# Kernel optimization log

Measured on AMD Instinct MI355X. Metric: run time of the kernel, lower is better.

Reference implementation:

```python
import jax, jax.numpy as jnp
import numpy as np

# Config mirroring MultiHeadAttention1d(in_channels=256, n_heads=8, residual=False,
# kernel_size=1, attention_type=0) applied to 3-D inputs (B, C, N).
B, C, N, H, D = 4, 256, 2048, 8, 256  # per-head dim D = in_channels; OC = H*D = 2048
OC = H * D


def setup_inputs() -> dict:
    key = jax.random.key(0)
    ks = jax.random.split(key, 14)
    s = 1.0 / np.sqrt(C)
    f32 = jnp.float32
    inp = {
        "x": jax.random.normal(ks[0], (B, C, N), f32),
        "y": jax.random.normal(ks[1], (B, C, N), f32),
        # ConvNormActivation1d (kernel_size=1) == pointwise conv + (folded, eval-mode)
        # BatchNorm affine + ReLU. BN folds to per-channel scale g and shift beta.
        "Wq": jax.random.normal(ks[2], (OC, C), f32) * s,
        "bq": jax.random.normal(ks[3], (OC,), f32) * 0.01,
        "gq": jnp.ones((OC,), f32),
        "betaq": jnp.zeros((OC,), f32),
        "Wk": jax.random.normal(ks[4], (OC, C), f32) * s,
        "bk": jax.random.normal(ks[5], (OC,), f32) * 0.01,
        "gk": jnp.ones((OC,), f32),
        "betak": jnp.zeros((OC,), f32),
        "Wv": jax.random.normal(ks[6], (OC, C), f32) * s,
        "bv": jax.random.normal(ks[7], (OC,), f32) * 0.01,
        "gv": jnp.ones((OC,), f32),
        "betav": jnp.zeros((OC,), f32),
    }
    return inp


def _cna(W, b, g, beta, t):
    # 1x1 conv (channel GEMM) + folded-BN affine + ReLU; t: (B, C, N) -> (B, OC, N)
    z = jnp.einsum("oc,bcn->bon", W, t) + b[:, None]
    return jax.nn.relu(g[:, None] * z + beta[:, None])


def _heads(t):
    # (B, OC, N) -> (B, H, N, D); channel split matches torch.split chunks of size D
    return t.reshape(B, H, D, N).transpose(0, 1, 3, 2)


def reference(x, y, Wq, bq, gq, betaq, Wk, bk, gk, betak, Wv, bv, gv, betav):
    q = _heads(_cna(Wq, bq, gq, betaq, x))  # (B,H,N,D)
    k = _heads(_cna(Wk, bk, gk, betak, y))
    v = _heads(_cna(Wv, bv, gv, betav, y))
    energy = jnp.einsum("bhnd,bhmd->bhnm", q, k)  # bmm(Q, K^T)
    attn = jax.nn.softmax(energy, axis=-1)
    out = jnp.einsum("bhnm,bhmd->bhnd", attn, v)  # (B,H,N,D)
    # torch path: view(H,B,k,N,D).permute(1,0,3,2,4) -> (B,H,N,k=1,D);
    # squeeze(dim=2) is a no-op since N != 1.
    return out[:, :, :, None, :]  # (B, H, N, 1, D)
```

## Files before the change

kernel.cpp:

```cpp
#include <hip/hip_runtime.h>
#include <cstdint>
#include <cstddef>

typedef unsigned short u16;
typedef __attribute__((ext_vector_type(4))) float f32x4;
typedef __attribute__((ext_vector_type(16))) float f32x16;
typedef __attribute__((ext_vector_type(8))) _Float16 f16x8;
typedef __attribute__((ext_vector_type(4))) u16   u16x4;
typedef __attribute__((ext_vector_type(8))) u16   u16x8;
typedef __attribute__((ext_vector_type(4))) int   i32x4;

#define DEV static __device__ __forceinline__
#define MFMA16(a,b,c) __builtin_amdgcn_mfma_f32_16x16x32_f16((a),(b),(c),0,0,0)
#define MFMA32(a,b,c) __builtin_amdgcn_mfma_f32_32x32x16_f16((a),(b),(c),0,0,0)

constexpr int Bc = 4, Cc = 256, Nc = 2048, Hc = 8, Dc = 256, OCc = 2048;

constexpr size_t OFF_XT = 0;
constexpr size_t OFF_YT = OFF_XT + (size_t)Bc*Nc*Cc*2;
constexpr size_t OFF_WQ = OFF_YT + (size_t)Bc*Nc*Cc*2;
constexpr size_t OFF_WK = OFF_WQ + (size_t)OCc*Cc*2;
constexpr size_t OFF_WV = OFF_WK + (size_t)OCc*Cc*2;
constexpr size_t OFF_BQ = OFF_WV + (size_t)OCc*Cc*2;
constexpr size_t OFF_BK = OFF_BQ + (size_t)OCc*4;
constexpr size_t OFF_BV = OFF_BK + (size_t)OCc*4;
constexpr size_t OFF_Q  = OFF_BV + (size_t)OCc*4;
constexpr size_t OFF_K  = OFF_Q  + (size_t)Bc*Hc*Nc*Dc*2;
constexpr size_t OFF_V  = OFF_K  + (size_t)Bc*Hc*Nc*Dc*2;

DEV u16 f2h(float x){
  _Float16 h = (_Float16)x;
  return __builtin_bit_cast(u16, h);
}

DEV void load_lds16(const void* g, void* l){
  __builtin_amdgcn_global_load_lds((const __attribute__((address_space(1))) int*)g,
                                   (__attribute__((address_space(3))) int*)l, 16, 0, 0);
}

__global__ __launch_bounds__(256) void transpose_cast(const float* __restrict__ x,
                                                      const float* __restrict__ y,
                                                      u16* __restrict__ XT,
                                                      u16* __restrict__ YT){
  __shared__ u16 tile[64][65];
  int b = blockIdx.z >> 1;
  const float* src = (blockIdx.z & 1) ? y : x;
  u16* dst = (blockIdx.z & 1) ? YT : XT;
  int n0 = blockIdx.x * 64, c0 = blockIdx.y * 64;
  int t = threadIdx.x;
#pragma unroll
  for (int i = 0; i < 16; ++i){
    int slot = i*256 + t;
    int cl = slot >> 6, nl = slot & 63;
    tile[cl][nl] = f2h(src[((size_t)b*Cc + c0 + cl)*Nc + n0 + nl]);
  }
  __syncthreads();
#pragma unroll
  for (int i = 0; i < 8; ++i){
    int slot = i*256 + t;
    int nl = slot >> 5, cl = (slot & 31)*2;
    uint32_t v = (uint32_t)tile[cl][nl] | ((uint32_t)tile[cl+1][nl] << 16);
    *(uint32_t*)(dst + ((size_t)b*Nc + n0 + nl)*Cc + c0 + cl) = v;
  }
}

__global__ __launch_bounds__(256) void prep_w(const float* __restrict__ W,
                                              const float* __restrict__ bsrc,
                                              const float* __restrict__ g,
                                              const float* __restrict__ beta,
                                              u16* __restrict__ Wo,
                                              float* __restrict__ bb){
  int idx = (blockIdx.x*256 + threadIdx.x) * 8;
  int o = idx >> 8, c = idx & 255;
  float gg = g[o];
  f32x4 a0 = *(const f32x4*)(W + idx);
  f32x4 a1 = *(const f32x4*)(W + idx + 4);
  u16x8 r;
#pragma unroll
  for (int i = 0; i < 4; ++i){ r[i] = f2h(a0[i]*gg); r[i+4] = f2h(a1[i]*gg); }
  *(u16x8*)(Wo + idx) = r;
  if (c == 0) bb[o] = gg*bsrc[o] + beta[o];
}

template<int SW>
__global__ __launch_bounds__(256, 2) void proj_gemm(const u16* __restrict__ Xt,
                                                    const u16* __restrict__ Wp,
                                                    const float* __restrict__ bb,
                                                    u16* __restrict__ outp){
  __shared__ __align__(16) char lds[32768];
  int t = threadIdx.x, w = t >> 6, l = t & 63, q = l & 15, g = l >> 4;
  int b = blockIdx.z;
  int n0 = blockIdx.x * 128, o0 = blockIdx.y * 128;
  int fs = ((q >> 1) & 3) << 4;
  int partg = ((l & 3) ^ ((l >> 3) & 3));
  f32x4 acc[4][4] = {};

  for (int it = 0; it < 4; ++it){
    __syncthreads();
#pragma unroll
    for (int j = 0; j < 8; ++j){
      int s = j*4 + w;
      int chunk = s >> 3;
      int off = (s & 7) * 1024;
      int row = (s & 7)*16 + (l >> 2);
      const char* gsrc;
      if (chunk < 2)
        gsrc = (const char*)(Wp + (size_t)(o0 + row)*Cc) + it*128 + chunk*64 + partg*16;
      else
        gsrc = (const char*)(Xt + ((size_t)b*Nc + n0 + row)*Cc) + it*128 + (chunk & 1)*64 + partg*16;
      load_lds16(gsrc, lds + chunk*8192 + off);
    }
    asm volatile("s_waitcnt vmcnt(0)" ::: "memory");
    __syncthreads();
#pragma unroll
    for (int kc = 0; kc < 2; ++kc){
      f16x8 fw[4], fx[4];
#pragma unroll
      for (int i = 0; i < 4; ++i){
        int wrow = (SW ? (w & 1) : (w >> 1))*64 + i*16 + q;
        int xrow = (SW ? (w >> 1) : (w & 1))*64 + i*16 + q;
        fw[i] = *(const f16x8*)(lds + kc*8192 + wrow*64 + ((g*16) ^ fs));
        fx[i] = *(const f16x8*)(lds + 16384 + kc*8192 + xrow*64 + ((g*16) ^ fs));
      }
#pragma unroll
      for (int i = 0; i < 4; ++i)
#pragma unroll
        for (int jj = 0; jj < 4; ++jj){
          if constexpr (!SW) acc[i][jj] = MFMA16(fw[i], fx[jj], acc[i][jj]);
          else               acc[i][jj] = MFMA16(fx[i], fw[jj], acc[i][jj]);
        }
    }
  }

  if constexpr (!SW) {
    f32x4 bias[4];
#pragma unroll
    for (int i = 0; i < 4; ++i) bias[i] = *(const f32x4*)(bb + o0 + (w>>1)*64 + i*16 + 4*g);
#pragma unroll
    for (int i = 0; i < 4; ++i)
#pragma unroll
      for (int jj = 0; jj < 4; ++jj){
        u16x4 pk;
#pragma unroll
        for (int r = 0; r < 4; ++r){
          float z = acc[i][jj][r] + bias[i][r];
          pk[r] = f2h(fmaxf(z, 0.f));
        }
        int o = o0 + (w>>1)*64 + i*16 + 4*g;
        int n = n0 + (w&1)*64 + jj*16 + q;
        int hh = o >> 8, d = o & 255;
        *(u16x4*)(outp + ((size_t)((b*Hc + hh)*Nc + n))*Dc + d) = pk;
      }
  } else {
    float biasv[4];
#pragma unroll
    for (int i = 0; i < 4; ++i) biasv[i] = bb[o0 + (w&1)*64 + i*16 + q];
#pragma unroll
    for (int i = 0; i < 4; ++i)
#pragma unroll
      for (int jj = 0; jj < 4; ++jj){
        u16x4 pk;
#pragma unroll
        for (int r = 0; r < 4; ++r){
          float z = acc[i][jj][r] + biasv[jj];
          pk[r] = f2h(fmaxf(z, 0.f));
        }
        int o = o0 + (w&1)*64 + jj*16 + q;
        int n = n0 + (w>>1)*64 + i*16 + 4*g;
        int hh = o >> 8, d = o & 255;
        *(u16x4*)(outp + ((size_t)((b*Hc + hh)*Dc + d))*Nc + n) = pk;
      }
  }
}

__global__ __launch_bounds__(512, 1) void attn_kernel(const u16* __restrict__ Qp,
                                                      const u16* __restrict__ Kp,
                                                      const u16* __restrict__ Vp,
                                                      float* __restrict__ outp){
  __shared__ __align__(16) char lds[150528];
  const int t = threadIdx.x, w = t >> 6, l = t & 63, lq = l & 31, hi = l >> 5;
  const int wq = w & 3, wm = w >> 2;
  const int h = blockIdx.y, b = blockIdx.z;
  const int q0 = blockIdx.x * 128;
  size_t head = (size_t)(b*Hc + h) * Nc * Dc;
  const u16* Qh = Qp + head;
  const u16* Kh = Kp + head;
  const u16* Vh = Vp + head;

  char* Pex  = lds + 131072;
  float* smax = (float*)(lds + 147456);
  float* ssum = (float*)(lds + 148480);
  float* sscl = (float*)(lds + 149504);
  float* slinv= (float*)(lds + 150016);

  f16x8 qf[16];
  {
    const u16* qrow = Qh + (size_t)(q0 + wq*32 + lq) * Dc;
#pragma unroll
    for (int kc = 0; kc < 16; ++kc) qf[kc] = *(const f16x8*)(qrow + kc*16 + hi*8);
  }

  f32x16 acc[4] = {};
  float m_run = -1e30f, l_run = 0.f;

#define STAGE_KV(m0_, buf_)                                                        \
  {                                                                                \
    char* Kd = lds + (buf_)*32768;                                                 \
    char* Vd = lds + 65536 + (buf_)*32768;                                         \
    _Pragma("unroll")                                                              \
    for (int j = 0; j < 4; ++j){                                                   \
      int row = w*8 + j*2 + hi;                                                    \
      int gs = (l & 31) ^ (row & 31);                                              \
      load_lds16(Kh + (size_t)((m0_) + row)*Dc + gs*8, Kd + w*4096 + j*1024);      \
    }                                                                              \
    _Pragma("unroll")                                                              \
    for (int j = 0; j < 4; ++j){                                                   \
      int ri = w*4 + j;                                                            \
      int r512 = 2*ri + (l >> 5);                                                  \
      int d = r512*4 + ((l >> 3) & 3);                                             \
      int m16 = (l & 7) ^ (r512 & 7);                                              \
      load_lds16(Vh + (size_t)d*Nc + (m0_) + m16*8, Vd + ri*1024);                 \
    }                                                                              \
  }

  STAGE_KV(0, 0);
  asm volatile("s_waitcnt vmcnt(0)" ::: "memory");
  __syncthreads();

  for (int it = 0; it < 32; ++it){
    const int cur = it & 1;
    char* Kc = lds + cur*32768;
    char* Vc = lds + 65536 + cur*32768;

    if (it < 31) STAGE_KV((it + 1)*64, cur ^ 1);

    f32x16 s = {};
    __builtin_amdgcn_s_setprio(1);
#pragma unroll
    for (int kc = 0; kc < 16; ++kc){
      f16x8 kf = *(const f16x8*)(Kc + (wm*32 + lq)*512 + (((kc*2 + hi) ^ lq) << 4));
      s = MFMA32(kf, qf[kc], s);
    }
    __builtin_amdgcn_s_setprio(0);

    float tmax = s[0];
#pragma unroll
    for (int r = 1; r < 16; ++r) tmax = fmaxf(tmax, s[r]);
    tmax = fmaxf(tmax, __shfl_xor(tmax, 32));
    if (!hi) smax[(wq*2 + wm)*32 + lq] = tmax;
    __syncthreads();
    float omax = smax[(wq*2 + (1 - wm))*32 + lq];
    float mnew = fmaxf(m_run, fmaxf(tmax, omax));
    float scale = __expf(m_run - mnew);

    float p[16];
    float rsum = 0.f;
#pragma unroll
    for (int r = 0; r < 16; ++r){ p[r] = __expf(s[r] - mnew); rsum += p[r]; }
    rsum += __shfl_xor(rsum, 32);
    if (!hi){
      ssum[(wq*2 + wm)*32 + lq] = rsum;
      if (!wm) sscl[wq*32 + lq] = scale;
    }

    int pk[8];
#pragma unroll
    for (int j2 = 0; j2 < 8; ++j2)
      pk[j2] = __builtin_bit_cast(int, __builtin_amdgcn_cvt_pkrtz(p[2*j2], p[2*j2+1]));
    int sx[8];
#pragma unroll
    for (int j2 = 0; j2 < 8; ++j2) sx[j2] = __shfl_xor(pk[j2], 32);
    i32x4 f0, f1;
    f0[0] = hi ? sx[2] : pk[0];  f0[1] = hi ? sx[3] : pk[1];
    f0[2] = hi ? pk[2] : sx[0];  f0[3] = hi ? pk[3] : sx[1];
    f1[0] = hi ? sx[6] : pk[4];  f1[1] = hi ? sx[7] : pk[5];
    f1[2] = hi ? pk[6] : sx[4];  f1[3] = hi ? pk[7] : sx[5];
    *(i32x4*)(Pex + w*2048 + l*16)        = f0;
    *(i32x4*)(Pex + w*2048 + 1024 + l*16) = f1;
    __syncthreads();

    float osum = ssum[(wq*2 + (1 - wm))*32 + lq];
    l_run = l_run * scale + rsum + osum;
    m_run = mnew;

    float sc[16];
#pragma unroll
    for (int r = 0; r < 16; ++r) sc[r] = sscl[wq*32 + (r & 3) + 8*(r >> 2) + 4*hi];
#pragma unroll
    for (int dt = 0; dt < 4; ++dt)
#pragma unroll
      for (int r = 0; r < 16; ++r) acc[dt][r] *= sc[r];

    i32x4 g0 = *(const i32x4*)(Pex + (w ^ 4)*2048 + l*16);
    i32x4 g1 = *(const i32x4*)(Pex + (w ^ 4)*2048 + 1024 + l*16);
    f16x8 a0 = __builtin_bit_cast(f16x8, wm ? g0 : f0);
    f16x8 a1 = __builtin_bit_cast(f16x8, wm ? g1 : f1);
    f16x8 a2 = __builtin_bit_cast(f16x8, wm ? f0 : g0);
    f16x8 a3 = __builtin_bit_cast(f16x8, wm ? f1 : g1);

    __builtin_amdgcn_s_setprio(1);
#pragma unroll
    for (int h2 = 0; h2 < 2; ++h2)
#pragma unroll
      for (int dt = 0; dt < 4; ++dt)
#pragma unroll
        for (int mcl = 0; mcl < 2; ++mcl){
          f16x8 vf = *(const f16x8*)(Vc + (wm*32 + dt*8 + (lq >> 2))*512 +
                                     (((lq & 3)*8 + ((h2*4 + mcl*2 + hi) ^ (lq >> 2)))*16));
          f16x8 af = h2 ? (mcl ? a3 : a2) : (mcl ? a1 : a0);
          acc[dt] = MFMA32(af, vf, acc[dt]);
        }
    __builtin_amdgcn_s_setprio(0);

    asm volatile("s_waitcnt vmcnt(0)" ::: "memory");
    __syncthreads();
  }
#undef STAGE_KV

  if (!hi && !wm) slinv[wq*32 + lq] = 1.f / l_run;
  __syncthreads();
  float li[16];
#pragma unroll
  for (int r = 0; r < 16; ++r) li[r] = slinv[wq*32 + (r & 3) + 8*(r >> 2) + 4*hi];
#pragma unroll
  for (int dt = 0; dt < 4; ++dt)
#pragma unroll
    for (int r = 0; r < 16; ++r){
      int qrow_ = wq*32 + (r & 3) + 8*(r >> 2) + 4*hi;
      int d = wm*128 + dt*32 + lq;
      outp[head + (size_t)(q0 + qrow_)*Dc + d] = acc[dt][r] * li[r];
    }
}

extern "C" void kernel_launch(void* const* d_in, const int* in_sizes, int n_in,
                              void* d_out, int out_size, void* d_ws, size_t ws_size,
                              hipStream_t stream){
  const float* x     = (const float*)d_in[0];
  const float* y     = (const float*)d_in[1];
  const float* Wq    = (const float*)d_in[2];
  const float* bq    = (const float*)d_in[3];
  const float* gq    = (const float*)d_in[4];
  const float* betaq = (const float*)d_in[5];
  const float* Wk    = (const float*)d_in[6];
  const float* bk    = (const float*)d_in[7];
  const float* gk    = (const float*)d_in[8];
  const float* betak = (const float*)d_in[9];
  const float* Wv    = (const float*)d_in[10];
  const float* bv    = (const float*)d_in[11];
  const float* gv    = (const float*)d_in[12];
  const float* betav = (const float*)d_in[13];
  char* ws = (char*)d_ws;
  float* outp = (float*)d_out;

  u16* XT = (u16*)(ws + OFF_XT);
  u16* YT = (u16*)(ws + OFF_YT);
  u16* WQb = (u16*)(ws + OFF_WQ);
  u16* WKb = (u16*)(ws + OFF_WK);
  u16* WVb = (u16*)(ws + OFF_WV);
  float* BQ = (float*)(ws + OFF_BQ);
  float* BK = (float*)(ws + OFF_BK);
  float* BV = (float*)(ws + OFF_BV);
  u16* Qw = (u16*)(ws + OFF_Q);
  u16* Kw = (u16*)(ws + OFF_K);
  u16* Vw = (u16*)(ws + OFF_V);

  transpose_cast<<<dim3(Nc/64, Cc/64, Bc*2), 256, 0, stream>>>(x, y, XT, YT);
  prep_w<<<dim3(OCc*Cc/2048), 256, 0, stream>>>(Wq, bq, gq, betaq, WQb, BQ);
  prep_w<<<dim3(OCc*Cc/2048), 256, 0, stream>>>(Wk, bk, gk, betak, WKb, BK);
  prep_w<<<dim3(OCc*Cc/2048), 256, 0, stream>>>(Wv, bv, gv, betav, WVb, BV);

  dim3 pg(Nc/128, OCc/128, Bc);
  proj_gemm<0><<<pg, 256, 0, stream>>>(XT, WQb, BQ, Qw);
  proj_gemm<0><<<pg, 256, 0, stream>>>(YT, WKb, BK, Kw);
  proj_gemm<1><<<pg, 256, 0, stream>>>(YT, WVb, BV, Vw);

  attn_kernel<<<dim3(Nc/128, Hc, Bc), 512, 0, stream>>>(Qw, Kw, Vw, outp);
}
```

Before: 272.6 us.

## Shrink attention blocks to 64 queries and single-buffer K/V for two blocks per CU

The attention kernel goes from 512-thread blocks of 128 queries to 256-thread blocks of 64 queries, and LDS use drops by half so two blocks can share a CU. K/V staging changes from double buffering to a single buffer. The next K tile is loaded after the QK^T MMAs and the next V tile after the PV MMAs, with vmcnt waits placed so each load overlaps the other phase's compute. The V LDS layout loses its XOR swizzle, which may add bank conflicts. The smaller blocks also re-read K/V twice as often from global memory.

New measurement: 312.3 us. 1.15x slower.

```diff
diff --git a/kernel.cpp b/kernel.cpp
--- a/kernel.cpp
+++ b/kernel.cpp
@@ -173,25 +173,27 @@
   }
 }
 
-__global__ __launch_bounds__(512, 1) void attn_kernel(const u16* __restrict__ Qp,
+__global__ __launch_bounds__(256, 2) void attn_kernel(const u16* __restrict__ Qp,
                                                       const u16* __restrict__ Kp,
                                                       const u16* __restrict__ Vp,
                                                       float* __restrict__ outp){
-  __shared__ __align__(16) char lds[150528];
+  __shared__ __align__(16) char lds[75264];
   const int t = threadIdx.x, w = t >> 6, l = t & 63, lq = l & 31, hi = l >> 5;
-  const int wq = w & 3, wm = w >> 2;
+  const int wq = w & 1, wm = w >> 1;
   const int h = blockIdx.y, b = blockIdx.z;
-  const int q0 = blockIdx.x * 128;
+  const int q0 = blockIdx.x * 64;
   size_t head = (size_t)(b*Hc + h) * Nc * Dc;
   const u16* Qh = Qp + head;
   const u16* Kh = Kp + head;
   const u16* Vh = Vp + head;
 
-  char* Pex  = lds + 131072;
-  float* smax = (float*)(lds + 147456);
-  float* ssum = (float*)(lds + 148480);
-  float* sscl = (float*)(lds + 149504);
-  float* slinv= (float*)(lds + 150016);
+  char* Kl = lds;
+  char* Vl = lds + 32768;
+  char* Pex  = lds + 65536;
+  float* smax = (float*)(lds + 73728);
+  float* ssum = (float*)(lds + 74240);
+  float* sscl = (float*)(lds + 74752);
+  float* slinv= (float*)(lds + 75008);
 
   f16x8 qf[16];
   {
@@ -203,42 +205,41 @@
   f32x16 acc[4] = {};
   float m_run = -1e30f, l_run = 0.f;
 
-#define STAGE_KV(m0_, buf_)                                                        \
+#define STAGE_K(m0_)                                                               \
   {                                                                                \
-    char* Kd = lds + (buf_)*32768;                                                 \
-    char* Vd = lds + 65536 + (buf_)*32768;                                         \
     _Pragma("unroll")                                                              \
-    for (int j = 0; j < 4; ++j){                                                   \
-      int row = w*8 + j*2 + hi;                                                    \
+    for (int j = 0; j < 8; ++j){                                                   \
+      int row = w*16 + j*2 + hi;                                                   \
       int gs = (l & 31) ^ (row & 31);                                              \
-      load_lds16(Kh + (size_t)((m0_) + row)*Dc + gs*8, Kd + w*4096 + j*1024);      \
+      load_lds16(Kh + (size_t)((m0_) + row)*Dc + gs*8, Kl + w*8192 + j*1024);      \
     }                                                                              \
+  }
+#define STAGE_V(m0_)                                                               \
+  {                                                                                \
     _Pragma("unroll")                                                              \
-    for (int j = 0; j < 4; ++j){                                                   \
-      int ri = w*4 + j;                                                            \
-      int r512 = 2*ri + (l >> 5);                                                  \
-      int d = r512*4 + ((l >> 3) & 3);                                             \
-      int m16 = (l & 7) ^ (r512 & 7);                                              \
-      load_lds16(Vh + (size_t)d*Nc + (m0_) + m16*8, Vd + ri*1024);                 \
+    for (int j = 0; j < 8; ++j){                                                   \
+      int rr = w*8 + j;                                                            \
+      int r512 = rr*2 + hi;                                                        \
+      int d = r512*4 + (l & 3);                                                    \
+      int m16 = (l >> 2) & 7;                                                      \
+      load_lds16(Vh + (size_t)d*Nc + (m0_) + m16*8, Vl + rr*1024);                 \
     }                                                                              \
   }
 
-  STAGE_KV(0, 0);
-  asm volatile("s_waitcnt vmcnt(0)" ::: "memory");
+  STAGE_K(0);
+  STAGE_V(0);
+  asm volatile("s_waitcnt vmcnt(8)" ::: "memory");
   __syncthreads();
 
   for (int it = 0; it < 32; ++it){
-    const int cur = it & 1;
-    char* Kc = lds + cur*32768;
-    char* Vc = lds + 65536 + cur*32768;
-
-    if (it < 31) STAGE_KV((it + 1)*64, cur ^ 1);
+    const int m0 = it * 64;
+    const int mn = (it < 31) ? (it + 1)*64 : it*64;
 
     f32x16 s = {};
     __builtin_amdgcn_s_setprio(1);
 #pragma unroll
     for (int kc = 0; kc < 16; ++kc){
-      f16x8 kf = *(const f16x8*)(Kc + (wm*32 + lq)*512 + (((kc*2 + hi) ^ lq) << 4));
+      f16x8 kf = *(const f16x8*)(Kl + (wm*32 + lq)*512 + (((kc*2 + hi) ^ lq) << 4));
       s = MFMA32(kf, qf[kc], s);
     }
     __builtin_amdgcn_s_setprio(0);
@@ -249,6 +250,9 @@
     tmax = fmaxf(tmax, __shfl_xor(tmax, 32));
     if (!hi) smax[(wq*2 + wm)*32 + lq] = tmax;
     __syncthreads();
+
+    STAGE_K(mn);
+
     float omax = smax[(wq*2 + (1 - wm))*32 + lq];
     float mnew = fmaxf(m_run, fmaxf(tmax, omax));
     float scale = __expf(m_run - mnew);
@@ -277,6 +281,8 @@
     f1[2] = hi ? pk[6] : sx[4];  f1[3] = hi ? pk[7] : sx[5];
     *(i32x4*)(Pex + w*2048 + l*16)        = f0;
     *(i32x4*)(Pex + w*2048 + 1024 + l*16) = f1;
+
+    asm volatile("s_waitcnt vmcnt(8)" ::: "memory");
     __syncthreads();
 
     float osum = ssum[(wq*2 + (1 - wm))*32 + lq];
@@ -291,8 +297,8 @@
 #pragma unroll
       for (int r = 0; r < 16; ++r) acc[dt][r] *= sc[r];
 
-    i32x4 g0 = *(const i32x4*)(Pex + (w ^ 4)*2048 + l*16);
-    i32x4 g1 = *(const i32x4*)(Pex + (w ^ 4)*2048 + 1024 + l*16);
+    i32x4 g0 = *(const i32x4*)(Pex + (w ^ 2)*2048 + l*16);
+    i32x4 g1 = *(const i32x4*)(Pex + (w ^ 2)*2048 + 1024 + l*16);
     f16x8 a0 = __builtin_bit_cast(f16x8, wm ? g0 : f0);
     f16x8 a1 = __builtin_bit_cast(f16x8, wm ? g1 : f1);
     f16x8 a2 = __builtin_bit_cast(f16x8, wm ? f0 : g0);
@@ -305,18 +311,22 @@
       for (int dt = 0; dt < 4; ++dt)
 #pragma unroll
         for (int mcl = 0; mcl < 2; ++mcl){
-          f16x8 vf = *(const f16x8*)(Vc + (wm*32 + dt*8 + (lq >> 2))*512 +
-                                     (((lq & 3)*8 + ((h2*4 + mcl*2 + hi) ^ (lq >> 2)))*16));
+          f16x8 vf = *(const f16x8*)(Vl + (wm*32 + dt*8 + (lq >> 2))*512 +
+                                     (((h2*4 + mcl*2 + hi)*4 + (lq & 3)) << 4));
           f16x8 af = h2 ? (mcl ? a3 : a2) : (mcl ? a1 : a0);
           acc[dt] = MFMA32(af, vf, acc[dt]);
         }
     __builtin_amdgcn_s_setprio(0);
 
-    asm volatile("s_waitcnt vmcnt(0)" ::: "memory");
-    __syncthreads();
-  }
-#undef STAGE_KV
-
+    __syncthreads();
+    STAGE_V(mn);
+    asm volatile("s_waitcnt vmcnt(8)" ::: "memory");
+    __syncthreads();
+  }
+#undef STAGE_K
+#undef STAGE_V
+
+  asm volatile("s_waitcnt vmcnt(0)" ::: "memory");
   if (!hi && !wm) slinv[wq*32 + lq] = 1.f / l_run;
   __syncthreads();
   float li[16];
@@ -374,5 +384,5 @@
   proj_gemm<0><<<pg, 256, 0, stream>>>(YT, WKb, BK, Kw);
   proj_gemm<1><<<pg, 256, 0, stream>>>(YT, WVb, BV, Vw);
 
-  attn_kernel<<<dim3(Nc/128, Hc, Bc), 512, 0, stream>>>(Qw, Kw, Vw, outp);
-}
+  attn_kernel<<<dim3(Nc/64, Hc, Bc), 256, 0, stream>>>(Qw, Kw, Vw, outp);
+}
```
